# Optimization experiments

Measured on AMD Instinct MI355X. Metric: run time of the kernel, lower is better.

Reference implementation:

```python
import jax, jax.numpy as jnp
import numpy as np

NUM_HEADS = 32
HEAD_DIM = 128
HEAVY_BUDGET = 256
RECENT_BUDGET = 256
ROPE_BASE = 10000.0


def _rope_tables(position_ids, head_dim, dtype):
    inv_freq = 1.0 / (ROPE_BASE ** (jnp.arange(0, head_dim, 2, dtype=jnp.float32) / head_dim))
    freqs = position_ids.astype(jnp.float32)[..., None] * inv_freq  # [b, s, hd/2]
    emb = jnp.concatenate([freqs, freqs], axis=-1)                  # [b, s, hd]
    return jnp.cos(emb).astype(dtype), jnp.sin(emb).astype(dtype)


def _rotate_half(x):
    h = x.shape[-1] // 2
    return jnp.concatenate([-x[..., h:], x[..., :h]], axis=-1)


def setup_inputs() -> dict:
    key = jax.random.key(0)
    k1, k2, k3, k4, k5 = jax.random.split(key, 5)
    b, s, d = 1, 2048, 4096
    hidden_states = jax.random.normal(k1, (b, s, d), dtype=jnp.float32)
    # additive causal mask, as HF passes into forward
    neg = jnp.finfo(jnp.float32).min
    causal = jnp.tril(jnp.ones((s, s), dtype=bool))
    attention_mask = jnp.where(causal, 0.0, neg).astype(jnp.float32)[None, None]  # [1,1,s,s]
    position_ids = jnp.arange(s, dtype=jnp.int32)[None]  # [1, s]
    scale = 0.02
    Wq = jax.random.normal(k2, (d, d), dtype=jnp.float32) * scale
    Wk = jax.random.normal(k3, (d, d), dtype=jnp.float32) * scale
    Wv = jax.random.normal(k4, (d, d), dtype=jnp.float32) * scale
    Wo = jax.random.normal(k5, (d, d), dtype=jnp.float32) * scale
    return {"hidden_states": hidden_states, "attention_mask": attention_mask,
            "position_ids": position_ids, "Wq": Wq, "Wk": Wk, "Wv": Wv, "Wo": Wo}


def reference(hidden_states, attention_mask, position_ids, Wq, Wk, Wv, Wo):
    b, s, d = hidden_states.shape
    H, hd = NUM_HEADS, HEAD_DIM
    kv = s  # prefill: no past_key_value, masks reset

    # projections: nn.Linear(x) = x @ W.T
    q = (hidden_states @ Wq.T).reshape(b, s, H, hd).transpose(0, 2, 1, 3)  # [b,H,s,hd]
    k = (hidden_states @ Wk.T).reshape(b, s, H, hd).transpose(0, 2, 1, 3)
    v = (hidden_states @ Wv.T).reshape(b, s, H, hd).transpose(0, 2, 1, 3)

    cos, sin = _rope_tables(position_ids, hd, q.dtype)  # [b,s,hd]
    cos, sin = cos[:, None], sin[:, None]               # broadcast over heads
    q = q * cos + _rotate_half(q) * sin
    k = k * cos + _rotate_half(k) * sin

    attn = jnp.einsum('bhqd,bhkd->bhqk', q, k) / np.float32(np.sqrt(hd))
    neg = jnp.finfo(attn.dtype).min
    attn = jnp.maximum(attn + attention_mask, neg)
    # attention_masks_next is None on the first (prefill) call -> no multiplicative mask here
    attn = jax.nn.softmax(attn.astype(jnp.float32), axis=-1).astype(q.dtype)  # [b,H,s,kv]

    # running per-head score accumulation: sum over batch and query dims
    scores = attn.sum(axis=0).sum(axis=1)  # [H, kv]; previous_scores is None at prefill

    # heavy-hitter eviction mask for the next decode step (kv+1 columns)
    mask = jnp.ones((H, kv + 1), dtype=attn.dtype)
    # attn_tokens_all (=kv) > cache_budget, recent_budget > 0:
    mask = mask.at[:, :kv + 1 - RECENT_BUDGET].set(0.0)
    selected = scores[:, :kv - RECENT_BUDGET]                    # drop recent region
    _, keep_topk = jax.lax.top_k(selected, HEAVY_BUDGET)         # [H, heavy]
    mask = mask.at[jnp.arange(H)[:, None], keep_topk].set(1.0)   # scatter heavy hitters
    # torch aliasing: score_mask = attn_mask[:, :-1]; score_mask[:, -recent:] = 1 mutates attn_mask too
    mask = mask.at[:, kv - RECENT_BUDGET:kv].set(1.0)
    attention_masks_next = mask[None, :, None, :]                # [1,H,1,kv+1]
    previous_scores = scores * mask[:, :kv]                      # masked score state

    out = jnp.einsum('bhqk,bhkd->bhqd', attn, v)                 # [b,H,s,hd]
    out = out.transpose(0, 2, 1, 3).reshape(b, s, d) @ Wo.T
    return out, attention_masks_next, previous_scores
```

## Files before the change

### kernel.cpp

```cpp
#include <hip/hip_runtime.h>
#include <hip/hip_bf16.h>
#include <cmath>

#define S_LEN 2048
#define DMODEL 4096
#define NH 32
#define HDIM 128
#define HEAVY 256
#define RECENT 256
#define ATTN_SCALE 0.08838834764831845f
#define NEGBIG -3.0e38f
#define MB (1024ull * 1024ull)

typedef __attribute__((ext_vector_type(8))) short short8v;
typedef __attribute__((ext_vector_type(4))) short short4v;
typedef __attribute__((ext_vector_type(4))) float floatx4;

__device__ inline ushort f2bf(float x) {
  __hip_bfloat16 h = __float2bfloat16(x);
  return __builtin_bit_cast(ushort, h);
}
__device__ inline float bf2f(ushort u) {
  __hip_bfloat16 h = __builtin_bit_cast(__hip_bfloat16, u);
  return __bfloat162float(h);
}
struct Split3 {
  short a, b, c;
};
__device__ inline Split3 split3(float x) {
  Split3 o;
  ushort u1 = f2bf(x);
  float r1 = x - bf2f(u1);
  ushort u2 = f2bf(r1);
  float r2 = r1 - bf2f(u2);
  ushort u3 = f2bf(r2);
  o.a = (short)u1;
  o.b = (short)u2;
  o.c = (short)u3;
  return o;
}

__global__ __launch_bounds__(256) void gemm6(const float* __restrict__ A,
                                             const float* __restrict__ B,
                                             float* __restrict__ C, int M, int N, int K) {
  __shared__ short Aa[128 * 40], Ab[128 * 40], Ac[128 * 40];
  __shared__ short Ba[128 * 40], Bb[128 * 40], Bc[128 * 40];
  const int tid = threadIdx.x;
  const int w = tid >> 6, l = tid & 63, g = l >> 4, ln = l & 15;
  const int wm = w >> 1, wn = w & 1;
  const int row0 = blockIdx.y * 128, col0 = blockIdx.x * 128;
  floatx4 acc[4][4] = {};
  for (int k0 = 0; k0 < K; k0 += 32) {
    __syncthreads();
#pragma unroll
    for (int i = 0; i < 4; i++) {
      int id = tid + i * 256;
      int r = id >> 3, c4 = id & 7;
      float4 av = *reinterpret_cast<const float4*>(&A[(size_t)(row0 + r) * K + k0 + c4 * 4]);
      float4 bv = *reinterpret_cast<const float4*>(&B[(size_t)(col0 + r) * K + k0 + c4 * 4]);
      float af[4] = {av.x, av.y, av.z, av.w};
      float bf[4] = {bv.x, bv.y, bv.z, bv.w};
      short4v a1, a2, a3, b1, b2, b3;
#pragma unroll
      for (int j = 0; j < 4; j++) {
        Split3 sa = split3(af[j]);
        Split3 sb = split3(bf[j]);
        a1[j] = sa.a; a2[j] = sa.b; a3[j] = sa.c;
        b1[j] = sb.a; b2[j] = sb.b; b3[j] = sb.c;
      }
      int o = r * 40 + c4 * 4;
      *reinterpret_cast<short4v*>(&Aa[o]) = a1;
      *reinterpret_cast<short4v*>(&Ab[o]) = a2;
      *reinterpret_cast<short4v*>(&Ac[o]) = a3;
      *reinterpret_cast<short4v*>(&Ba[o]) = b1;
      *reinterpret_cast<short4v*>(&Bb[o]) = b2;
      *reinterpret_cast<short4v*>(&Bc[o]) = b3;
    }
    __syncthreads();
#pragma unroll
    for (int i = 0; i < 4; i++) {
      int ar = (wm * 64 + i * 16 + ln) * 40 + g * 8;
      short8v a1 = *reinterpret_cast<const short8v*>(&Aa[ar]);
      short8v a2 = *reinterpret_cast<const short8v*>(&Ab[ar]);
      short8v a3 = *reinterpret_cast<const short8v*>(&Ac[ar]);
#pragma unroll
      for (int j = 0; j < 4; j++) {
        int br = (wn * 64 + j * 16 + ln) * 40 + g * 8;
        short8v b1 = *reinterpret_cast<const short8v*>(&Ba[br]);
        short8v b2 = *reinterpret_cast<const short8v*>(&Bb[br]);
        short8v b3 = *reinterpret_cast<const short8v*>(&Bc[br]);
        acc[i][j] = __builtin_amdgcn_mfma_f32_16x16x32_bf16(a1, b1, acc[i][j], 0, 0, 0);
        acc[i][j] = __builtin_amdgcn_mfma_f32_16x16x32_bf16(a1, b2, acc[i][j], 0, 0, 0);
        acc[i][j] = __builtin_amdgcn_mfma_f32_16x16x32_bf16(a2, b1, acc[i][j], 0, 0, 0);
        acc[i][j] = __builtin_amdgcn_mfma_f32_16x16x32_bf16(a1, b3, acc[i][j], 0, 0, 0);
        acc[i][j] = __builtin_amdgcn_mfma_f32_16x16x32_bf16(a2, b2, acc[i][j], 0, 0, 0);
        acc[i][j] = __builtin_amdgcn_mfma_f32_16x16x32_bf16(a3, b1, acc[i][j], 0, 0, 0);
      }
    }
  }
#pragma unroll
  for (int i = 0; i < 4; i++)
#pragma unroll
    for (int j = 0; j < 4; j++)
#pragma unroll
      for (int r = 0; r < 4; r++)
        C[(size_t)(row0 + wm * 64 + i * 16 + g * 4 + r) * N + col0 + wn * 64 + j * 16 + ln] =
            acc[i][j][r];
}

__global__ __launch_bounds__(256) void gemm_bf1(const float* __restrict__ A,
                                                const float* __restrict__ B,
                                                float* __restrict__ C, int M, int N, int K) {
  __shared__ short Ah[128 * 40];
  __shared__ short Bh[128 * 40];
  const int tid = threadIdx.x;
  const int w = tid >> 6, l = tid & 63, g = l >> 4, ln = l & 15;
  const int wm = w >> 1, wn = w & 1;
  const int row0 = blockIdx.y * 128, col0 = blockIdx.x * 128;
  floatx4 acc[4][4] = {};
  for (int k0 = 0; k0 < K; k0 += 32) {
    __syncthreads();
#pragma unroll
    for (int i = 0; i < 4; i++) {
      int id = tid + i * 256;
      int r = id >> 3, c4 = id & 7;
      float4 av = *reinterpret_cast<const float4*>(&A[(size_t)(row0 + r) * K + k0 + c4 * 4]);
      float4 bv = *reinterpret_cast<const float4*>(&B[(size_t)(col0 + r) * K + k0 + c4 * 4]);
      short4v ah, bh;
      ah[0] = (short)f2bf(av.x); ah[1] = (short)f2bf(av.y);
      ah[2] = (short)f2bf(av.z); ah[3] = (short)f2bf(av.w);
      bh[0] = (short)f2bf(bv.x); bh[1] = (short)f2bf(bv.y);
      bh[2] = (short)f2bf(bv.z); bh[3] = (short)f2bf(bv.w);
      *reinterpret_cast<short4v*>(&Ah[r * 40 + c4 * 4]) = ah;
      *reinterpret_cast<short4v*>(&Bh[r * 40 + c4 * 4]) = bh;
    }
    __syncthreads();
#pragma unroll
    for (int i = 0; i < 4; i++) {
      short8v a = *reinterpret_cast<const short8v*>(&Ah[(wm * 64 + i * 16 + ln) * 40 + g * 8]);
#pragma unroll
      for (int j = 0; j < 4; j++) {
        short8v b = *reinterpret_cast<const short8v*>(&Bh[(wn * 64 + j * 16 + ln) * 40 + g * 8]);
        acc[i][j] = __builtin_amdgcn_mfma_f32_16x16x32_bf16(a, b, acc[i][j], 0, 0, 0);
      }
    }
  }
#pragma unroll
  for (int i = 0; i < 4; i++)
#pragma unroll
    for (int j = 0; j < 4; j++)
#pragma unroll
      for (int r = 0; r < 4; r++)
        C[(size_t)(row0 + wm * 64 + i * 16 + g * 4 + r) * N + col0 + wn * 64 + j * 16 + ln] =
            acc[i][j][r];
}

__global__ __launch_bounds__(256) void gemm_vbt(const float* __restrict__ A,
                                                const float* __restrict__ B,
                                                ushort* __restrict__ Vt, int M, int N, int K) {
  __shared__ short Ah[128 * 40];
  __shared__ short Bh[128 * 40];
  const int tid = threadIdx.x;
  const int w = tid >> 6, l = tid & 63, g = l >> 4, ln = l & 15;
  const int wm = w >> 1, wn = w & 1;
  const int row0 = blockIdx.y * 128, col0 = blockIdx.x * 128;
  floatx4 acc[4][4] = {};
  for (int k0 = 0; k0 < K; k0 += 32) {
    __syncthreads();
#pragma unroll
    for (int i = 0; i < 4; i++) {
      int id = tid + i * 256;
      int r = id >> 3, c4 = id & 7;
      float4 av = *reinterpret_cast<const float4*>(&A[(size_t)(row0 + r) * K + k0 + c4 * 4]);
      float4 bv = *reinterpret_cast<const float4*>(&B[(size_t)(col0 + r) * K + k0 + c4 * 4]);
      short4v ah, bh;
      ah[0] = (short)f2bf(av.x); ah[1] = (short)f2bf(av.y);
      ah[2] = (short)f2bf(av.z); ah[3] = (short)f2bf(av.w);
      bh[0] = (short)f2bf(bv.x); bh[1] = (short)f2bf(bv.y);
      bh[2] = (short)f2bf(bv.z); bh[3] = (short)f2bf(bv.w);
      *reinterpret_cast<short4v*>(&Ah[r * 40 + c4 * 4]) = ah;
      *reinterpret_cast<short4v*>(&Bh[r * 40 + c4 * 4]) = bh;
    }
    __syncthreads();
#pragma unroll
    for (int i = 0; i < 4; i++) {
      short8v a = *reinterpret_cast<const short8v*>(&Ah[(wm * 64 + i * 16 + ln) * 40 + g * 8]);
#pragma unroll
      for (int j = 0; j < 4; j++) {
        short8v b = *reinterpret_cast<const short8v*>(&Bh[(wn * 64 + j * 16 + ln) * 40 + g * 8]);
        acc[i][j] = __builtin_amdgcn_mfma_f32_16x16x32_bf16(a, b, acc[i][j], 0, 0, 0);
      }
    }
  }
#pragma unroll
  for (int i = 0; i < 4; i++)
#pragma unroll
    for (int j = 0; j < 4; j++) {
      short4v o;
#pragma unroll
      for (int r = 0; r < 4; r++) o[r] = (short)f2bf(acc[i][j][r]);
      size_t n = col0 + wn * 64 + j * 16 + ln;
      size_t m0 = row0 + wm * 64 + i * 16 + g * 4;
      *reinterpret_cast<short4v*>(&Vt[n * M + m0]) = o;
    }
}

__global__ void rope_convert(const float* __restrict__ Q, const float* __restrict__ K,
                             const int* __restrict__ pos, short* __restrict__ Qa,
                             short* __restrict__ Qb, short* __restrict__ Qc,
                             short* __restrict__ Ka, short* __restrict__ Kb,
                             short* __restrict__ Kc) {
  int idx = blockIdx.x * blockDim.x + threadIdx.x;
  if (idx >= S_LEN * 64) return;
  int d = idx & 63;
  int r = idx >> 6;
  float p = (float)pos[r];
  float invf = (float)pow(10000.0, -(double)(2 * d) / 128.0);
  float ang = p * invf;
  float c = cosf(ang), s = sinf(ang);
  for (int h = 0; h < NH; h++) {
    size_t base = (size_t)r * DMODEL + h * HDIM + d;
    float q1 = Q[base], q2 = Q[base + 64];
    float k1 = K[base], k2 = K[base + 64];
    float qa = q1 * c - q2 * s, qb = q2 * c + q1 * s;
    float ka = k1 * c - k2 * s, kb = k2 * c + k1 * s;
    Split3 t;
    t = split3(qa); Qa[base] = t.a; Qb[base] = t.b; Qc[base] = t.c;
    t = split3(qb); Qa[base + 64] = t.a; Qb[base + 64] = t.b; Qc[base + 64] = t.c;
    t = split3(ka); Ka[base] = t.a; Kb[base] = t.b; Kc[base] = t.c;
    t = split3(kb); Ka[base + 64] = t.a; Kb[base + 64] = t.b; Kc[base + 64] = t.c;
  }
}

#define KVB 32
#define KTILE_SH (KVB * 128)

__device__ __forceinline__ floatx4 qk6_tile(const short* KaS, const short* KbS,
                                            const short* KcS, const short8v q1[4],
                                            const short8v q2[4], const short8v q3[4],
                                            int krow, int g) {
  floatx4 sacc = {};
#pragma unroll
  for (int dc = 0; dc < 4; dc++) {
    int didx = krow * 128 + ((dc * 32 + g * 8) ^ ((krow & 7) << 3));
    short8v k1 = *reinterpret_cast<const short8v*>(&KaS[didx]);
    short8v k2 = *reinterpret_cast<const short8v*>(&KbS[didx]);
    short8v k3 = *reinterpret_cast<const short8v*>(&KcS[didx]);
    sacc = __builtin_amdgcn_mfma_f32_16x16x32_bf16(q1[dc], k1, sacc, 0, 0, 0);
    sacc = __builtin_amdgcn_mfma_f32_16x16x32_bf16(q1[dc], k2, sacc, 0, 0, 0);
    sacc = __builtin_amdgcn_mfma_f32_16x16x32_bf16(q2[dc], k1, sacc, 0, 0, 0);
    sacc = __builtin_amdgcn_mfma_f32_16x16x32_bf16(q1[dc], k3, sacc, 0, 0, 0);
    sacc = __builtin_amdgcn_mfma_f32_16x16x32_bf16(q2[dc], k2, sacc, 0, 0, 0);
    sacc = __builtin_amdgcn_mfma_f32_16x16x32_bf16(q3[dc], k1, sacc, 0, 0, 0);
  }
  return sacc;
}

__device__ __forceinline__ void stage_load(const short* __restrict__ Ka,
                                           const short* __restrict__ Kb,
                                           const short* __restrict__ Kc, int k0, int h, int tid,
                                           short8v sA[2], short8v sB[2], short8v sC[2]) {
#pragma unroll
  for (int i = 0; i < 2; i++) {
    int id = tid + i * 256;
    int r = id >> 4, c = id & 15;
    size_t goff = (size_t)(k0 + r) * DMODEL + h * HDIM + c * 8;
    sA[i] = *reinterpret_cast<const short8v*>(&Ka[goff]);
    sB[i] = *reinterpret_cast<const short8v*>(&Kb[goff]);
    sC[i] = *reinterpret_cast<const short8v*>(&Kc[goff]);
  }
}

__device__ __forceinline__ void stage_store(short* KaS, short* KbS, short* KcS, int tid,
                                            const short8v sA[2], const short8v sB[2],
                                            const short8v sC[2]) {
#pragma unroll
  for (int i = 0; i < 2; i++) {
    int id = tid + i * 256;
    int r = id >> 4, c = id & 15;
    int didx = r * 128 + ((c * 8) ^ ((r & 7) << 3));
    *reinterpret_cast<short8v*>(&KaS[didx]) = sA[i];
    *reinterpret_cast<short8v*>(&KbS[didx]) = sB[i];
    *reinterpret_cast<short8v*>(&KcS[didx]) = sC[i];
  }
}

__device__ void process_qblock(int qb, int h, const short* __restrict__ Qa,
                               const short* __restrict__ Qb, const short* __restrict__ Qc,
                               const short* __restrict__ Ka, const short* __restrict__ Kb,
                               const short* __restrict__ Kc, const ushort* __restrict__ Vt,
                               float* __restrict__ AO, float* __restrict__ sp4, short* KS0,
                               short* Ps, int tid, int w, int g, int ln) {
  const int q0 = qb * 64;
  const int qrow = q0 + w * 16 + ln;
  short8v q1[4], q2[4], q3[4];
#pragma unroll
  for (int dc = 0; dc < 4; dc++) {
    size_t off = (size_t)qrow * DMODEL + h * HDIM + dc * 32 + g * 8;
    q1[dc] = *reinterpret_cast<const short8v*>(&Qa[off]);
    q2[dc] = *reinterpret_cast<const short8v*>(&Qb[off]);
    q3[dc] = *reinterpret_cast<const short8v*>(&Qc[off]);
  }
  float m_r[4], l_r[4];
#pragma unroll
  for (int r = 0; r < 4; r++) { m_r[r] = NEGBIG; l_r[r] = 0.f; }
  const int nkt = 2 * qb + 2;
  short8v sA[2], sB[2], sC[2];

  stage_load(Ka, Kb, Kc, 0, h, tid, sA, sB, sC);
  stage_store(KS0 + 0, KS0 + KTILE_SH, KS0 + 2 * KTILE_SH, tid, sA, sB, sC);
  __syncthreads();
  for (int t = 0; t < nkt; t++) {
    const int k0 = t * KVB;
    const int cur = t & 1, nxt = cur ^ 1;
    const bool pre = (t + 1 < nkt);
    if (pre) stage_load(Ka, Kb, Kc, k0 + KVB, h, tid, sA, sB, sC);
    short* KaS = KS0 + cur * 3 * KTILE_SH;
    float sv[2][4];
#pragma unroll
    for (int ct = 0; ct < 2; ct++) {
      floatx4 sacc = qk6_tile(KaS, KaS + KTILE_SH, KaS + 2 * KTILE_SH, q1, q2, q3, ct * 16 + ln, g);
#pragma unroll
      for (int r = 0; r < 4; r++) {
        float s = sacc[r] * ATTN_SCALE;
        int key = k0 + ct * 16 + ln;
        int qq = q0 + w * 16 + g * 4 + r;
        sv[ct][r] = (key <= qq) ? s : NEGBIG;
      }
    }
#pragma unroll
    for (int r = 0; r < 4; r++) {
      float tmax = fmaxf(sv[0][r], sv[1][r]);
      tmax = fmaxf(tmax, __shfl_xor(tmax, 1));
      tmax = fmaxf(tmax, __shfl_xor(tmax, 2));
      tmax = fmaxf(tmax, __shfl_xor(tmax, 4));
      tmax = fmaxf(tmax, __shfl_xor(tmax, 8));
      float mnew = fmaxf(m_r[r], tmax);
      float ssum = __expf(sv[0][r] - mnew) + __expf(sv[1][r] - mnew);
      ssum += __shfl_xor(ssum, 1);
      ssum += __shfl_xor(ssum, 2);
      ssum += __shfl_xor(ssum, 4);
      ssum += __shfl_xor(ssum, 8);
      l_r[r] = l_r[r] * __expf(m_r[r] - mnew) + ssum;
      m_r[r] = mnew;
    }
    if (pre) {
      short* KaN = KS0 + nxt * 3 * KTILE_SH;
      stage_store(KaN, KaN + KTILE_SH, KaN + 2 * KTILE_SH, tid, sA, sB, sC);
    }
    __syncthreads();
  }
  float inv_l[4];
#pragma unroll
  for (int r = 0; r < 4; r++) inv_l[r] = 1.0f / l_r[r];

  floatx4 o[8] = {};
  stage_load(Ka, Kb, Kc, 0, h, tid, sA, sB, sC);
  stage_store(KS0 + 0, KS0 + KTILE_SH, KS0 + 2 * KTILE_SH, tid, sA, sB, sC);
  __syncthreads();
  for (int t = 0; t < nkt; t++) {
    const int k0 = t * KVB;
    const int cur = t & 1, nxt = cur ^ 1;
    const bool pre = (t + 1 < nkt);
    if (pre) stage_load(Ka, Kb, Kc, k0 + KVB, h, tid, sA, sB, sC);
    short* KaS = KS0 + cur * 3 * KTILE_SH;
    float pv[2][4];
#pragma unroll
    for (int ct = 0; ct < 2; ct++) {
      floatx4 sacc = qk6_tile(KaS, KaS + KTILE_SH, KaS + 2 * KTILE_SH, q1, q2, q3, ct * 16 + ln, g);
#pragma unroll
      for (int r = 0; r < 4; r++) {
        float s = sacc[r] * ATTN_SCALE;
        int key = k0 + ct * 16 + ln;
        int qq = q0 + w * 16 + g * 4 + r;
        s = (key <= qq) ? s : NEGBIG;
        pv[ct][r] = __expf(s - m_r[r]) * inv_l[r];
      }
    }
#pragma unroll
    for (int ct = 0; ct < 2; ct++) {
      float c2 = pv[ct][0] + pv[ct][1] + pv[ct][2] + pv[ct][3];
      c2 += __shfl_xor(c2, 16);
      c2 += __shfl_xor(c2, 32);
      if (g == 0) sp4[((size_t)(qb * 4 + w) * NH + h) * S_LEN + k0 + ct * 16 + ln] = c2;
    }
#pragma unroll
    for (int ct = 0; ct < 2; ct++)
#pragma unroll
      for (int r = 0; r < 4; r++) {
        int prow = g * 4 + r, pcol = ct * 16 + ln;
        Ps[w * 512 + prow * 32 + (pcol ^ (((prow >> 1) & 1) << 4))] = (short)f2bf(pv[ct][r]);
      }
    short8v pa = *reinterpret_cast<const short8v*>(
        &Ps[w * 512 + ln * 32 + ((g * 8) ^ (((ln >> 1) & 1) << 4))]);
#pragma unroll
    for (int ctd = 0; ctd < 8; ctd++) {
      size_t voff = ((size_t)h * HDIM + ctd * 16 + ln) * S_LEN + k0 + g * 8;
      short8v vb = *reinterpret_cast<const short8v*>(&Vt[voff]);
      o[ctd] = __builtin_amdgcn_mfma_f32_16x16x32_bf16(pa, vb, o[ctd], 0, 0, 0);
    }
    if (pre) {
      short* KaN = KS0 + nxt * 3 * KTILE_SH;
      stage_store(KaN, KaN + KTILE_SH, KaN + 2 * KTILE_SH, tid, sA, sB, sC);
    }
    __syncthreads();
  }
#pragma unroll
  for (int ctd = 0; ctd < 8; ctd++)
#pragma unroll
    for (int r = 0; r < 4; r++)
      AO[(size_t)(q0 + w * 16 + g * 4 + r) * DMODEL + h * HDIM + ctd * 16 + ln] = o[ctd][r];
}

__global__ __launch_bounds__(256) void attn_fused(
    const short* __restrict__ Qa, const short* __restrict__ Qb, const short* __restrict__ Qc,
    const short* __restrict__ Ka, const short* __restrict__ Kb, const short* __restrict__ Kc,
    const ushort* __restrict__ Vt, float* __restrict__ AO, float* __restrict__ sp4) {
  __shared__ short KS[2 * 3 * KTILE_SH];
  __shared__ short Ps[4 * 512];
  const int bid = blockIdx.x;
  const int pid = bid >> 5, h = bid & 31;
  const int tid = threadIdx.x;
  const int w = tid >> 6, l = tid & 63, g = l >> 4, ln = l & 15;
  (void)l;
  process_qblock(31 - pid, h, Qa, Qb, Qc, Ka, Kb, Kc, Vt, AO, sp4, KS, Ps, tid, w, g, ln);
  process_qblock(pid, h, Qa, Qb, Qc, Ka, Kb, Kc, Vt, AO, sp4, KS, Ps, tid, w, g, ln);
}

__global__ void reduce_scores(const float* __restrict__ sp4, float* __restrict__ scores) {
  int idx = blockIdx.x * blockDim.x + threadIdx.x;
  if (idx >= NH * S_LEN) return;
  int h = idx >> 11, k = idx & 2047;
  float s = 0.f;
  for (int j = 0; j < 128; j++) s += sp4[((size_t)j * NH + h) * S_LEN + k];
  scores[idx] = s;
}

__global__ __launch_bounds__(256) void topk_mask_kernel(const float* __restrict__ scores,
                                                        float* __restrict__ out_mask,
                                                        float* __restrict__ prev_scores) {
  const int h = blockIdx.x;
  __shared__ unsigned sb[S_LEN - RECENT];
  __shared__ int cnt_sh;
  const int NSEL = S_LEN - RECENT;
  const int tid = threadIdx.x;
  const float* sc = scores + (size_t)h * S_LEN;
  for (int i = tid; i < NSEL; i += 256) sb[i] = __float_as_uint(sc[i]);
  __syncthreads();
  unsigned prefix = 0u;
  for (int b = 31; b >= 0; b--) {
    unsigned cand = prefix | (1u << b);
    if (tid == 0) cnt_sh = 0;
    __syncthreads();
    int c = 0;
    for (int i = tid; i < NSEL; i += 256) c += (sb[i] >= cand) ? 1 : 0;
    atomicAdd(&cnt_sh, c);
    __syncthreads();
    if (cnt_sh >= HEAVY) prefix = cand;
    __syncthreads();
  }
  if (tid == 0) cnt_sh = 0;
  __syncthreads();
  int c = 0;
  for (int i = tid; i < NSEL; i += 256) c += (sb[i] > prefix) ? 1 : 0;
  atomicAdd(&cnt_sh, c);
  __syncthreads();
  const int c1 = cnt_sh;
  float* mrow = out_mask + (size_t)h * (S_LEN + 1);
  float* prow = prev_scores + (size_t)h * S_LEN;
  for (int j = NSEL + tid; j < S_LEN + 1; j += 256) mrow[j] = 1.0f;
  for (int k = NSEL + tid; k < S_LEN; k += 256) prow[k] = sc[k];
  for (int i = tid; i < NSEL; i += 256) {
    bool sel = sb[i] > prefix;
    mrow[i] = sel ? 1.f : 0.f;
    prow[i] = sel ? sc[i] : 0.f;
  }
  __syncthreads();
  if (tid == 0) {
    int need = HEAVY - c1;
    for (int i = 0; i < NSEL && need > 0; i++) {
      if (sb[i] == prefix) { mrow[i] = 1.f; prow[i] = sc[i]; need--; }
    }
  }
}

extern "C" void kernel_launch(void* const* d_in, const int* in_sizes, int n_in,
                              void* d_out, int out_size, void* d_ws, size_t ws_size,
                              hipStream_t stream) {
  const float* hidden = (const float*)d_in[0];
  const int* pos = (const int*)d_in[2];
  const float* Wq = (const float*)d_in[3];
  const float* Wk = (const float*)d_in[4];
  const float* Wv = (const float*)d_in[5];
  const float* Wo = (const float*)d_in[6];

  float* out0 = (float*)d_out;
  float* out_mask = out0 + (size_t)S_LEN * DMODEL;
  float* prev_scores = out_mask + (size_t)NH * (S_LEN + 1);

  char* ws = (char*)d_ws;
  float* Qf = (float*)(ws + 0 * MB);
  float* Kf = (float*)(ws + 32 * MB);
  ushort* Vt = (ushort*)(ws + 64 * MB);
  short* Qa = (short*)(ws + 80 * MB);
  short* Qb = (short*)(ws + 96 * MB);
  short* Qc = (short*)(ws + 112 * MB);
  short* Ka = (short*)(ws + 128 * MB);
  short* Kb = (short*)(ws + 144 * MB);
  short* Kc = (short*)(ws + 160 * MB);
  float* AO = Qf;
  float* sp4 = Kf;
  float* scores = (float*)(ws + 64 * MB);

  dim3 gg(DMODEL / 128, S_LEN / 128);
  gemm6<<<gg, 256, 0, stream>>>(hidden, Wq, Qf, S_LEN, DMODEL, DMODEL);
  gemm6<<<gg, 256, 0, stream>>>(hidden, Wk, Kf, S_LEN, DMODEL, DMODEL);
  gemm_vbt<<<gg, 256, 0, stream>>>(hidden, Wv, Vt, S_LEN, DMODEL, DMODEL);

  int rope_total = S_LEN * 64;
  rope_convert<<<(rope_total + 255) / 256, 256, 0, stream>>>(Qf, Kf, pos, Qa, Qb, Qc, Ka, Kb, Kc);

  hipError_t _e = hipMemsetAsync(sp4, 0, (size_t)128 * NH * S_LEN * sizeof(float), stream);
  (void)_e;
  attn_fused<<<512, 256, 0, stream>>>(Qa, Qb, Qc, Ka, Kb, Kc, Vt, AO, sp4);

  reduce_scores<<<(NH * S_LEN + 255) / 256, 256, 0, stream>>>(sp4, scores);
  topk_mask_kernel<<<NH, 256, 0, stream>>>(scores, out_mask, prev_scores);

  gemm_bf1<<<gg, 256, 0, stream>>>(AO, Wo, out0, S_LEN, DMODEL, DMODEL);
}
```

Before: 1.763 ms.

## Pre-split inputs and weights into bf16 triples before Q/K/V projection GEMMs

Adds a split_mat kernel that converts hidden states and Wq/Wk into three bf16 components once, and a gemm6p GEMM that loads the pre-split shorts directly instead of splitting fp32 inside every tile load. The V projection reuses the pre-split hidden high part. The QK tile function now uses six independent accumulators so the MFMA chain can overlap. This removes redundant per-tile split arithmetic but adds extra global traffic and separate split passes, and only takes effect when the workspace is large enough.

```diff
diff --git a/kernel.cpp b/kernel.cpp
--- a/kernel.cpp
+++ b/kernel.cpp
@@ -40,6 +40,83 @@
   return o;
 }
 
+__global__ void split_mat(const float* __restrict__ X, short* __restrict__ Xa,
+                          short* __restrict__ Xb, short* __restrict__ Xc, int n4) {
+  int stride = gridDim.x * blockDim.x;
+  for (int i = blockIdx.x * blockDim.x + threadIdx.x; i < n4; i += stride) {
+    float4 v = reinterpret_cast<const float4*>(X)[i];
+    float vv[4] = {v.x, v.y, v.z, v.w};
+    short4v a, b, c;
+#pragma unroll
+    for (int j = 0; j < 4; j++) {
+      Split3 t = split3(vv[j]);
+      a[j] = t.a; b[j] = t.b; c[j] = t.c;
+    }
+    reinterpret_cast<short4v*>(Xa)[i] = a;
+    reinterpret_cast<short4v*>(Xb)[i] = b;
+    reinterpret_cast<short4v*>(Xc)[i] = c;
+  }
+}
+
+__global__ __launch_bounds__(256) void gemm6p(
+    const short* __restrict__ Aag, const short* __restrict__ Abg, const short* __restrict__ Acg,
+    const short* __restrict__ Bag, const short* __restrict__ Bbg, const short* __restrict__ Bcg,
+    float* __restrict__ C, int M, int N, int K) {
+  __shared__ short Aa[128 * 40], Ab[128 * 40], Ac[128 * 40];
+  __shared__ short Ba[128 * 40], Bb[128 * 40], Bc[128 * 40];
+  const int tid = threadIdx.x;
+  const int w = tid >> 6, l = tid & 63, g = l >> 4, ln = l & 15;
+  const int wm = w >> 1, wn = w & 1;
+  const int row0 = blockIdx.y * 128, col0 = blockIdx.x * 128;
+  floatx4 acc[4][4] = {};
+  for (int k0 = 0; k0 < K; k0 += 32) {
+    __syncthreads();
+#pragma unroll
+    for (int i = 0; i < 2; i++) {
+      int id = tid + i * 256;
+      int r = id >> 2, c = id & 3;
+      size_t ga = (size_t)(row0 + r) * K + k0 + c * 8;
+      size_t gb = (size_t)(col0 + r) * K + k0 + c * 8;
+      int o = r * 40 + c * 8;
+      *reinterpret_cast<short8v*>(&Aa[o]) = *reinterpret_cast<const short8v*>(&Aag[ga]);
+      *reinterpret_cast<short8v*>(&Ab[o]) = *reinterpret_cast<const short8v*>(&Abg[ga]);
+      *reinterpret_cast<short8v*>(&Ac[o]) = *reinterpret_cast<const short8v*>(&Acg[ga]);
+      *reinterpret_cast<short8v*>(&Ba[o]) = *reinterpret_cast<const short8v*>(&Bag[gb]);
+      *reinterpret_cast<short8v*>(&Bb[o]) = *reinterpret_cast<const short8v*>(&Bbg[gb]);
+      *reinterpret_cast<short8v*>(&Bc[o]) = *reinterpret_cast<const short8v*>(&Bcg[gb]);
+    }
+    __syncthreads();
+#pragma unroll
+    for (int i = 0; i < 4; i++) {
+      int ar = (wm * 64 + i * 16 + ln) * 40 + g * 8;
+      short8v a1 = *reinterpret_cast<const short8v*>(&Aa[ar]);
+      short8v a2 = *reinterpret_cast<const short8v*>(&Ab[ar]);
+      short8v a3 = *reinterpret_cast<const short8v*>(&Ac[ar]);
+#pragma unroll
+      for (int j = 0; j < 4; j++) {
+        int br = (wn * 64 + j * 16 + ln) * 40 + g * 8;
+        short8v b1 = *reinterpret_cast<const short8v*>(&Ba[br]);
+        short8v b2 = *reinterpret_cast<const short8v*>(&Bb[br]);
+        short8v b3 = *reinterpret_cast<const short8v*>(&Bc[br]);
+        acc[i][j] = __builtin_amdgcn_mfma_f32_16x16x32_bf16(a1, b1, acc[i][j], 0, 0, 0);
+        acc[i][j] = __builtin_amdgcn_mfma_f32_16x16x32_bf16(a1, b2, acc[i][j], 0, 0, 0);
+        acc[i][j] = __builtin_amdgcn_mfma_f32_16x16x32_bf16(a2, b1, acc[i][j], 0, 0, 0);
+        acc[i][j] = __builtin_amdgcn_mfma_f32_16x16x32_bf16(a1, b3, acc[i][j], 0, 0, 0);
+        acc[i][j] = __builtin_amdgcn_mfma_f32_16x16x32_bf16(a2, b2, acc[i][j], 0, 0, 0);
+        acc[i][j] = __builtin_amdgcn_mfma_f32_16x16x32_bf16(a3, b1, acc[i][j], 0, 0, 0);
+      }
+    }
+  }
+#pragma unroll
+  for (int i = 0; i < 4; i++)
+#pragma unroll
+    for (int j = 0; j < 4; j++)
+#pragma unroll
+      for (int r = 0; r < 4; r++)
+        C[(size_t)(row0 + wm * 64 + i * 16 + g * 4 + r) * N + col0 + wn * 64 + j * 16 + ln] =
+            acc[i][j][r];
+}
+
 __global__ __launch_bounds__(256) void gemm6(const float* __restrict__ A,
                                              const float* __restrict__ B,
                                              float* __restrict__ C, int M, int N, int K) {
@@ -155,7 +232,8 @@
             acc[i][j][r];
 }
 
-__global__ __launch_bounds__(256) void gemm_vbt(const float* __restrict__ A,
+template <int AK>
+__global__ __launch_bounds__(256) void gemm_vbt(const void* __restrict__ Av,
                                                 const float* __restrict__ B,
                                                 ushort* __restrict__ Vt, int M, int N, int K) {
   __shared__ short Ah[128 * 40];
@@ -167,18 +245,32 @@
   floatx4 acc[4][4] = {};
   for (int k0 = 0; k0 < K; k0 += 32) {
     __syncthreads();
+    if (AK) {
+      const short* Ab = (const short*)Av;
+#pragma unroll
+      for (int i = 0; i < 2; i++) {
+        int id = tid + i * 256;
+        int r = id >> 2, c = id & 3;
+        *reinterpret_cast<short8v*>(&Ah[r * 40 + c * 8]) =
+            *reinterpret_cast<const short8v*>(&Ab[(size_t)(row0 + r) * K + k0 + c * 8]);
+      }
+    }
 #pragma unroll
     for (int i = 0; i < 4; i++) {
       int id = tid + i * 256;
       int r = id >> 3, c4 = id & 7;
-      float4 av = *reinterpret_cast<const float4*>(&A[(size_t)(row0 + r) * K + k0 + c4 * 4]);
+      if (!AK) {
+        const float* Af = (const float*)Av;
+        float4 av = *reinterpret_cast<const float4*>(&Af[(size_t)(row0 + r) * K + k0 + c4 * 4]);
+        short4v ah;
+        ah[0] = (short)f2bf(av.x); ah[1] = (short)f2bf(av.y);
+        ah[2] = (short)f2bf(av.z); ah[3] = (short)f2bf(av.w);
+        *reinterpret_cast<short4v*>(&Ah[r * 40 + c4 * 4]) = ah;
+      }
       float4 bv = *reinterpret_cast<const float4*>(&B[(size_t)(col0 + r) * K + k0 + c4 * 4]);
-      short4v ah, bh;
-      ah[0] = (short)f2bf(av.x); ah[1] = (short)f2bf(av.y);
-      ah[2] = (short)f2bf(av.z); ah[3] = (short)f2bf(av.w);
+      short4v bh;
       bh[0] = (short)f2bf(bv.x); bh[1] = (short)f2bf(bv.y);
       bh[2] = (short)f2bf(bv.z); bh[3] = (short)f2bf(bv.w);
-      *reinterpret_cast<short4v*>(&Ah[r * 40 + c4 * 4]) = ah;
       *reinterpret_cast<short4v*>(&Bh[r * 40 + c4 * 4]) = bh;
     }
     __syncthreads();
@@ -239,21 +331,21 @@
                                             const short* KcS, const short8v q1[4],
                                             const short8v q2[4], const short8v q3[4],
                                             int krow, int g) {
-  floatx4 sacc = {};
+  floatx4 cA = {}, cB = {}, cC = {}, cD = {}, cE = {}, cF = {};
 #pragma unroll
   for (int dc = 0; dc < 4; dc++) {
     int didx = krow * 128 + ((dc * 32 + g * 8) ^ ((krow & 7) << 3));
     short8v k1 = *reinterpret_cast<const short8v*>(&KaS[didx]);
     short8v k2 = *reinterpret_cast<const short8v*>(&KbS[didx]);
     short8v k3 = *reinterpret_cast<const short8v*>(&KcS[didx]);
-    sacc = __builtin_amdgcn_mfma_f32_16x16x32_bf16(q1[dc], k1, sacc, 0, 0, 0);
-    sacc = __builtin_amdgcn_mfma_f32_16x16x32_bf16(q1[dc], k2, sacc, 0, 0, 0);
-    sacc = __builtin_amdgcn_mfma_f32_16x16x32_bf16(q2[dc], k1, sacc, 0, 0, 0);
-    sacc = __builtin_amdgcn_mfma_f32_16x16x32_bf16(q1[dc], k3, sacc, 0, 0, 0);
-    sacc = __builtin_amdgcn_mfma_f32_16x16x32_bf16(q2[dc], k2, sacc, 0, 0, 0);
-    sacc = __builtin_amdgcn_mfma_f32_16x16x32_bf16(q3[dc], k1, sacc, 0, 0, 0);
-  }
-  return sacc;
+    cA = __builtin_amdgcn_mfma_f32_16x16x32_bf16(q1[dc], k1, cA, 0, 0, 0);
+    cB = __builtin_amdgcn_mfma_f32_16x16x32_bf16(q1[dc], k2, cB, 0, 0, 0);
+    cC = __builtin_amdgcn_mfma_f32_16x16x32_bf16(q2[dc], k1, cC, 0, 0, 0);
+    cD = __builtin_amdgcn_mfma_f32_16x16x32_bf16(q1[dc], k3, cD, 0, 0, 0);
+    cE = __builtin_amdgcn_mfma_f32_16x16x32_bf16(q2[dc], k2, cE, 0, 0, 0);
+    cF = __builtin_amdgcn_mfma_f32_16x16x32_bf16(q3[dc], k1, cF, 0, 0, 0);
+  }
+  return ((cA + cB) + (cC + cD)) + (cE + cF);
 }
 
 __device__ __forceinline__ void stage_load(const short* __restrict__ Ka,
@@ -513,9 +605,25 @@
   float* scores = (float*)(ws + 64 * MB);
 
   dim3 gg(DMODEL / 128, S_LEN / 128);
-  gemm6<<<gg, 256, 0, stream>>>(hidden, Wq, Qf, S_LEN, DMODEL, DMODEL);
-  gemm6<<<gg, 256, 0, stream>>>(hidden, Wk, Kf, S_LEN, DMODEL, DMODEL);
-  gemm_vbt<<<gg, 256, 0, stream>>>(hidden, Wv, Vt, S_LEN, DMODEL, DMODEL);
+  const bool big = ws_size >= 224 * MB;
+  if (big) {
+    short* Wsa = (short*)(ws + 80 * MB);
+    short* Wsb = (short*)(ws + 112 * MB);
+    short* Wsc = (short*)(ws + 144 * MB);
+    short* Ha = (short*)(ws + 176 * MB);
+    short* Hb = (short*)(ws + 192 * MB);
+    short* Hc = (short*)(ws + 208 * MB);
+    split_mat<<<2048, 256, 0, stream>>>(hidden, Ha, Hb, Hc, S_LEN * DMODEL / 4);
+    split_mat<<<2048, 256, 0, stream>>>(Wq, Wsa, Wsb, Wsc, DMODEL * DMODEL / 4);
+    gemm6p<<<gg, 256, 0, stream>>>(Ha, Hb, Hc, Wsa, Wsb, Wsc, Qf, S_LEN, DMODEL, DMODEL);
+    split_mat<<<2048, 256, 0, stream>>>(Wk, Wsa, Wsb, Wsc, DMODEL * DMODEL / 4);
+    gemm6p<<<gg, 256, 0, stream>>>(Ha, Hb, Hc, Wsa, Wsb, Wsc, Kf, S_LEN, DMODEL, DMODEL);
+    gemm_vbt<1><<<gg, 256, 0, stream>>>(Ha, Wv, Vt, S_LEN, DMODEL, DMODEL);
+  } else {
+    gemm6<<<gg, 256, 0, stream>>>(hidden, Wq, Qf, S_LEN, DMODEL, DMODEL);
+    gemm6<<<gg, 256, 0, stream>>>(hidden, Wk, Kf, S_LEN, DMODEL, DMODEL);
+    gemm_vbt<0><<<gg, 256, 0, stream>>>(hidden, Wv, Vt, S_LEN, DMODEL, DMODEL);
+  }
 
   int rope_total = S_LEN * 64;
   rope_convert<<<(rope_total + 255) / 256, 256, 0, stream>>>(Qf, Kf, pos, Qa, Qb, Qc, Ka, Kb, Kc);
```

Result: slower. 1.870 ms (+6.1%).
